# Kernel tuning notes

Measured on AMD Instinct MI355X. Metric: run time of the kernel, lower is better.

## Reference

```python
import jax, jax.numpy as jnp
import numpy as np
import math

HIDDEN = 128

def setup_inputs() -> dict:
    key = jax.random.key(0)
    k1, k2, k3 = jax.random.split(key, 3)
    X = jax.random.normal(k1, (4, 4096, HIDDEN), dtype=jnp.float32)
    # nn.Linear(hidden, 3*hidden): weight [3H, H], bias [3H]
    bound = 1.0 / math.sqrt(HIDDEN)
    W = jax.random.uniform(k2, (3 * HIDDEN, HIDDEN), minval=-bound, maxval=bound, dtype=jnp.float32)
    b = jax.random.uniform(k3, (3 * HIDDEN,), minval=-bound, maxval=bound, dtype=jnp.float32)
    return {"X": X, "W": W, "b": b}

def reference(X, W, b):
    H = X.shape[-1]
    # fused QKV projection: X @ W^T + b -> [B, S, 3H]
    qkv = jnp.einsum('bsh,oh->bso', X, W) + b
    Q, K, V = jnp.split(qkv, 3, axis=-1)
    # scaled dot-product attention (single head)
    scores = jnp.einsum('bqh,bkh->bqk', Q, K) / jnp.sqrt(jnp.asarray(H, X.dtype))
    weights = jax.nn.softmax(scores, axis=-1)
    return jnp.einsum('bqk,bkh->bqh', weights, V)
```

## Files before the change

### kernel.cpp

```cpp
#include <hip/hip_runtime.h>
#include <hip/hip_fp16.h>

typedef _Float16 f16;
typedef __attribute__((ext_vector_type(8))) _Float16 f16x8;
typedef __attribute__((ext_vector_type(4))) float f32x4;
typedef __attribute__((ext_vector_type(4))) unsigned int u32x4;
typedef __attribute__((ext_vector_type(2))) unsigned int u32x2;

#define BB 4
#define SS 4096
#define HH 128
#define SC2 0.12752462157076558f

union H2U { __half2 h; unsigned int u; };
union VU { u32x4 v; unsigned short s[8]; };
union F8U { u32x4 u; f16x8 h; };

#define LW 136
__global__ __launch_bounds__(256) void qkv_gemm(
    const float* __restrict__ X, const float* __restrict__ W,
    const float* __restrict__ bias, f16* __restrict__ Qh,
    f16* __restrict__ Kh, f16* __restrict__ Vh)
{
    __shared__ f16 sW[64 * LW];
    const int bx = blockIdx.x, by = blockIdx.y;
    const int t = threadIdx.x;
    const int w = t >> 6, lane = t & 63;
    const int c = lane & 15, quad = lane >> 4;

    f16x8 af[2][4];
    const int rbase = bx * 128 + w * 32;
#pragma unroll
    for (int mt = 0; mt < 2; ++mt) {
        const float* xr = X + (size_t)(rbase + mt * 16 + c) * HH + quad * 8;
#pragma unroll
        for (int kc = 0; kc < 4; ++kc) {
            float4 a = *(const float4*)(xr + kc * 32);
            float4 b = *(const float4*)(xr + kc * 32 + 4);
            H2U u0, u1, u2, u3;
            u0.h = __floats2half2_rn(a.x, a.y);
            u1.h = __floats2half2_rn(a.z, a.w);
            u2.h = __floats2half2_rn(b.x, b.y);
            u3.h = __floats2half2_rn(b.z, b.w);
            F8U pk; pk.u.x = u0.u; pk.u.y = u1.u; pk.u.z = u2.u; pk.u.w = u3.u;
            af[mt][kc] = pk.h;
        }
    }

    {
        const int r = t >> 2, q = t & 3;
        const float* src = W + (size_t)(by * 64 + r) * HH + q * 32;
        f16* dst = sW + r * LW + q * 32;
#pragma unroll
        for (int i = 0; i < 8; ++i) {
            float4 v = ((const float4*)src)[i];
            __half2 a = __floats2half2_rn(v.x, v.y);
            __half2 b = __floats2half2_rn(v.z, v.w);
            ((__half2*)dst)[2 * i] = a;
            ((__half2*)dst)[2 * i + 1] = b;
        }
    }
    __syncthreads();

    f32x4 acc[2][4];
#pragma unroll
    for (int mt = 0; mt < 2; ++mt)
#pragma unroll
        for (int nt = 0; nt < 4; ++nt) acc[mt][nt] = (f32x4)0.f;

#pragma unroll
    for (int kc = 0; kc < 4; ++kc) {
        f16x8 bf[4];
#pragma unroll
        for (int nt = 0; nt < 4; ++nt)
            bf[nt] = *(const f16x8*)&sW[(nt * 16 + c) * LW + kc * 32 + quad * 8];
#pragma unroll
        for (int mt = 0; mt < 2; ++mt)
#pragma unroll
            for (int nt = 0; nt < 4; ++nt)
                acc[mt][nt] = __builtin_amdgcn_mfma_f32_16x16x32_f16(af[mt][kc], bf[nt], acc[mt][nt], 0, 0, 0);
    }

    f16* outp = (by < 2) ? Qh : (by < 4) ? Kh : Vh;
    const int cbase = (by & 1) * 64;
#pragma unroll
    for (int nt = 0; nt < 4; ++nt) {
        const int cc = cbase + nt * 16 + c;
        const float bv = bias[by * 64 + nt * 16 + c];
#pragma unroll
        for (int mt = 0; mt < 2; ++mt) {
#pragma unroll
            for (int r = 0; r < 4; ++r) {
                const int row = rbase + mt * 16 + quad * 4 + r;
                outp[(size_t)row * HH + cc] = (f16)(acc[mt][nt][r] + bv);
            }
        }
    }
}

#define BM 64
#define BN 64
#define LK 136
#define LV 88
#define LP 88

__global__ __launch_bounds__(128, 2) void attn_mfma(
    const f16* __restrict__ Qh, const f16* __restrict__ Kh,
    const f16* __restrict__ Vh, float* __restrict__ out,
    float* __restrict__ Opart, float2* __restrict__ ml, int nsplit)
{
    __shared__ f16 sK[BN * LK];
    __shared__ f16 sVt[HH * LV];
    __shared__ f16 sP[2][32 * LP];

    const int bid = blockIdx.x;
    const int split = bid >> 8;
    const int inner = bid & 255;
    const int batch = inner & 3;
    const int qtile = inner >> 2;
    const int t = threadIdx.x;
    const int w = t >> 6, lane = t & 63;
    const int c = lane & 15, quad = lane >> 4;

    const int s0 = (64 * split) / nsplit;
    const int s1 = (64 * (split + 1)) / nsplit;
    const int nst = s1 - s0;
    const int kstart = s0 * BN;

    const f16* Qb = Qh + (size_t)batch * SS * HH;
    const f16* Kb = Kh + (size_t)batch * SS * HH;
    const f16* Vb = Vh + (size_t)batch * SS * HH;
    const int qbase = qtile * BM + w * 32;

    f16x8 qf[2][4];
#pragma unroll
    for (int qt = 0; qt < 2; ++qt)
#pragma unroll
        for (int kc = 0; kc < 4; ++kc)
            qf[qt][kc] = *(const f16x8*)(Qb + (size_t)(qbase + qt * 16 + c) * HH + kc * 32 + quad * 8);

    const int kr = t >> 1, kh = t & 1;
    const f16* kgp = Kb + (size_t)(kstart + kr) * HH + kh * 64;
    f16* ksp = sK + kr * LK + kh * 64;
    const int vkp = t & 31, vhq = t >> 5;
    const f16* vgp = Vb + (size_t)(kstart + 2 * vkp) * HH;

    u32x4 kbuf[8], vb0[4], vb1[4];
#pragma unroll
    for (int i = 0; i < 8; ++i) kbuf[i] = *(const u32x4*)(kgp + i * 8);
#pragma unroll
    for (int p = 0; p < 4; ++p) {
        const int hg = vhq * 4 + p;
        vb0[p] = *(const u32x4*)(vgp + hg * 8);
        vb1[p] = *(const u32x4*)(vgp + HH + hg * 8);
    }

    f32x4 oacc[2][8];
#pragma unroll
    for (int mt = 0; mt < 2; ++mt)
#pragma unroll
        for (int nt = 0; nt < 8; ++nt) oacc[mt][nt] = (f32x4)0.f;
    float m_[2] = {-1e30f, -1e30f}, l_[2] = {0.f, 0.f};

    for (int st = 0; st < nst; ++st) {
        __syncthreads();
#pragma unroll
        for (int i = 0; i < 8; ++i) *(u32x4*)(ksp + i * 8) = kbuf[i];
#pragma unroll
        for (int p = 0; p < 4; ++p) {
            const int hg = vhq * 4 + p;
            VU a, b; a.v = vb0[p]; b.v = vb1[p];
#pragma unroll
            for (int i = 0; i < 8; ++i) {
                unsigned int pk = (unsigned int)a.s[i] | ((unsigned int)b.s[i] << 16);
                *(unsigned int*)&sVt[(hg * 8 + i) * LV + 2 * vkp] = pk;
            }
        }
        __syncthreads();
        if (st + 1 < nst) {
            const f16* kg = kgp + (size_t)(st + 1) * BN * HH;
#pragma unroll
            for (int i = 0; i < 8; ++i) kbuf[i] = *(const u32x4*)(kg + i * 8);
            const f16* vg = vgp + (size_t)(st + 1) * BN * HH;
#pragma unroll
            for (int p = 0; p < 4; ++p) {
                const int hg = vhq * 4 + p;
                vb0[p] = *(const u32x4*)(vg + hg * 8);
                vb1[p] = *(const u32x4*)(vg + HH + hg * 8);
            }
        }

        f32x4 sacc[4][2];
#pragma unroll
        for (int km = 0; km < 4; ++km)
#pragma unroll
            for (int qt = 0; qt < 2; ++qt) sacc[km][qt] = (f32x4)0.f;
#pragma unroll
        for (int kc = 0; kc < 4; ++kc) {
#pragma unroll
            for (int km = 0; km < 4; ++km) {
                f16x8 kf = *(const f16x8*)&sK[(km * 16 + c) * LK + kc * 32 + quad * 8];
#pragma unroll
                for (int qt = 0; qt < 2; ++qt)
                    sacc[km][qt] = __builtin_amdgcn_mfma_f32_16x16x32_f16(kf, qf[qt][kc], sacc[km][qt], 0, 0, 0);
            }
        }

        float alpha_s[2];
#pragma unroll
        for (int qt = 0; qt < 2; ++qt) {
            float mx = sacc[0][qt][0];
#pragma unroll
            for (int km = 0; km < 4; ++km)
#pragma unroll
                for (int r = 0; r < 4; ++r) mx = fmaxf(mx, sacc[km][qt][r]);
            mx = fmaxf(mx, __shfl_xor(mx, 16));
            mx = fmaxf(mx, __shfl_xor(mx, 32));
            const float mn = fmaxf(m_[qt], mx);
            const float alpha = exp2f((m_[qt] - mn) * SC2);
            m_[qt] = mn;
            alpha_s[qt] = alpha;
            const float tb = mn * SC2;
            float ls = 0.f;
#pragma unroll
            for (int km = 0; km < 4; ++km) {
                float p0 = exp2f(sacc[km][qt][0] * SC2 - tb);
                float p1 = exp2f(sacc[km][qt][1] * SC2 - tb);
                float p2 = exp2f(sacc[km][qt][2] * SC2 - tb);
                float p3 = exp2f(sacc[km][qt][3] * SC2 - tb);
                ls += (p0 + p1) + (p2 + p3);
                H2U u0, u1;
                u0.h = __floats2half2_rn(p0, p1);
                u1.h = __floats2half2_rn(p2, p3);
                u32x2 pk; pk.x = u0.u; pk.y = u1.u;
                *(u32x2*)&sP[w][(qt * 16 + c) * LP + km * 16 + quad * 4] = pk;
            }
            ls += __shfl_xor(ls, 16);
            ls += __shfl_xor(ls, 32);
            l_[qt] = l_[qt] * alpha + ls;
        }

#pragma unroll
        for (int mt = 0; mt < 2; ++mt) {
            float av[4];
#pragma unroll
            for (int r = 0; r < 4; ++r)
                av[r] = __shfl(alpha_s[mt], quad * 4 + r);
#pragma unroll
            for (int nt = 0; nt < 8; ++nt)
#pragma unroll
                for (int r = 0; r < 4; ++r) oacc[mt][nt][r] *= av[r];
        }

#pragma unroll
        for (int kc2 = 0; kc2 < 2; ++kc2) {
            f16x8 pf[2];
#pragma unroll
            for (int mt = 0; mt < 2; ++mt)
                pf[mt] = *(const f16x8*)&sP[w][(mt * 16 + c) * LP + kc2 * 32 + quad * 8];
#pragma unroll
            for (int nt = 0; nt < 8; ++nt) {
                f16x8 vf = *(const f16x8*)&sVt[(nt * 16 + c) * LV + kc2 * 32 + quad * 8];
#pragma unroll
                for (int mt = 0; mt < 2; ++mt)
                    oacc[mt][nt] = __builtin_amdgcn_mfma_f32_16x16x32_f16(pf[mt], vf, oacc[mt][nt], 0, 0, 0);
            }
        }
    }

    float* Ob = (split == 0) ? out : (Opart + (size_t)(split - 1) * BB * SS * HH);
    float* ob = Ob + (size_t)(batch * SS + qbase) * HH;
    if (nsplit == 1) {
#pragma unroll
        for (int mt = 0; mt < 2; ++mt) {
            float lv[4];
#pragma unroll
            for (int r = 0; r < 4; ++r)
                lv[r] = 1.f / __shfl(l_[mt], quad * 4 + r);
#pragma unroll
            for (int r = 0; r < 4; ++r) {
                const int row = mt * 16 + quad * 4 + r;
#pragma unroll
                for (int nt = 0; nt < 8; ++nt)
                    ob[(size_t)row * HH + nt * 16 + c] = oacc[mt][nt][r] * lv[r];
            }
        }
    } else {
#pragma unroll
        for (int mt = 0; mt < 2; ++mt) {
#pragma unroll
            for (int r = 0; r < 4; ++r) {
                const int row = mt * 16 + quad * 4 + r;
#pragma unroll
                for (int nt = 0; nt < 8; ++nt)
                    ob[(size_t)row * HH + nt * 16 + c] = oacc[mt][nt][r];
            }
        }
        if (quad == 0) {
#pragma unroll
            for (int qt = 0; qt < 2; ++qt) {
                float2 v; v.x = m_[qt]; v.y = l_[qt];
                ml[((size_t)split * BB + batch) * SS + qbase + qt * 16 + c] = v;
            }
        }
    }
}

__global__ __launch_bounds__(256) void attn_merge(
    float* __restrict__ out, const float* __restrict__ Opart,
    const float2* __restrict__ ml, int nsplit)
{
    const int idx = blockIdx.x * 256 + threadIdx.x;
    const int chunk = idx & 31;
    const int q = (idx >> 5) & (SS - 1);
    const int b = idx >> 17;
    float m = -1e30f;
    for (int s = 0; s < nsplit; ++s)
        m = fmaxf(m, ml[((size_t)s * BB + b) * SS + q].x);
    float L = 0.f;
    float ax = 0.f, ay = 0.f, az = 0.f, aw = 0.f;
    for (int s = 0; s < nsplit; ++s) {
        float2 v = ml[((size_t)s * BB + b) * SS + q];
        const float wgt = exp2f((v.x - m) * SC2);
        L += v.y * wgt;
        const float* Op = (s == 0) ? out : (Opart + (size_t)(s - 1) * BB * SS * HH);
        float4 o = *(const float4*)(Op + ((size_t)b * SS + q) * HH + chunk * 4);
        ax += wgt * o.x; ay += wgt * o.y; az += wgt * o.z; aw += wgt * o.w;
    }
    const float inv = 1.f / L;
    float4 r; r.x = ax * inv; r.y = ay * inv; r.z = az * inv; r.w = aw * inv;
    *(float4*)(out + ((size_t)b * SS + q) * HH + chunk * 4) = r;
}

extern "C" void kernel_launch(void* const* d_in, const int* in_sizes, int n_in,
                              void* d_out, int out_size, void* d_ws, size_t ws_size,
                              hipStream_t stream) {
    const float* X = (const float*)d_in[0];
    const float* W = (const float*)d_in[1];
    const float* bias = (const float*)d_in[2];
    float* out = (float*)d_out;

    char* ws = (char*)d_ws;
    const size_t qkv_bytes = (size_t)3 * BB * SS * HH * sizeof(f16);
    const size_t o_bytes   = (size_t)BB * SS * HH * sizeof(float);
    const size_t ml_bytes  = (size_t)BB * SS * sizeof(float2);

    int S = 1;
    if (ws_size >= qkv_bytes + 2 * o_bytes + 3 * ml_bytes) S = 3;
    else if (ws_size >= qkv_bytes + 1 * o_bytes + 2 * ml_bytes) S = 2;

    f16* Qh = (f16*)ws;
    f16* Kh = Qh + (size_t)BB * SS * HH;
    f16* Vh = Kh + (size_t)BB * SS * HH;
    float* Opart = (float*)(ws + qkv_bytes);
    float2* ml = (float2*)(ws + qkv_bytes + (size_t)(S - 1) * o_bytes);

    qkv_gemm<<<dim3(128, 6), 256, 0, stream>>>(X, W, bias, Qh, Kh, Vh);
    attn_mfma<<<256 * S, 128, 0, stream>>>(Qh, Kh, Vh, out, Opart, ml, S);
    if (S > 1)
        attn_merge<<<BB * SS * (HH / 4) / 256, 256, 0, stream>>>(out, Opart, ml, S);
}
```

Before: 157.5 us.

## Enlarge attention query tile to 128 rows with 4 waves, widen QKV GEMM tile

The attention kernel now processes 128 query rows per block with 256 threads (four waves) instead of 64 rows with two waves. Each K/V tile staged in shared memory is therefore reused by twice as many queries, and the per-thread staging load is halved. The QKV GEMM block now computes a full 128-column output slice so X fragments are converted once per block instead of twice. The split-K count can rise to 4 to recover parallelism lost by the halved block count, at the cost of more partial output traffic in the merge step and higher shared memory per block.

Result: faster. 138.2 us (-12.3%).

```diff
diff --git a/kernel.cpp b/kernel.cpp
--- a/kernel.cpp
+++ b/kernel.cpp
@@ -22,7 +22,7 @@
     const float* __restrict__ bias, f16* __restrict__ Qh,
     f16* __restrict__ Kh, f16* __restrict__ Vh)
 {
-    __shared__ f16 sW[64 * LW];
+    __shared__ f16 sW[128 * LW];
     const int bx = blockIdx.x, by = blockIdx.y;
     const int t = threadIdx.x;
     const int w = t >> 6, lane = t & 63;
@@ -48,11 +48,11 @@
     }
 
     {
-        const int r = t >> 2, q = t & 3;
-        const float* src = W + (size_t)(by * 64 + r) * HH + q * 32;
-        f16* dst = sW + r * LW + q * 32;
-#pragma unroll
-        for (int i = 0; i < 8; ++i) {
+        const int r = t >> 1, h = t & 1;
+        const float* src = W + (size_t)(by * 128 + r) * HH + h * 64;
+        f16* dst = sW + r * LW + h * 64;
+#pragma unroll
+        for (int i = 0; i < 16; ++i) {
             float4 v = ((const float4*)src)[i];
             __half2 a = __floats2half2_rn(v.x, v.y);
             __half2 b = __floats2half2_rn(v.z, v.w);
@@ -62,31 +62,28 @@
     }
     __syncthreads();
 
-    f32x4 acc[2][4];
+    f32x4 acc[2][8];
 #pragma unroll
     for (int mt = 0; mt < 2; ++mt)
 #pragma unroll
-        for (int nt = 0; nt < 4; ++nt) acc[mt][nt] = (f32x4)0.f;
+        for (int nt = 0; nt < 8; ++nt) acc[mt][nt] = (f32x4)0.f;
 
 #pragma unroll
     for (int kc = 0; kc < 4; ++kc) {
-        f16x8 bf[4];
-#pragma unroll
-        for (int nt = 0; nt < 4; ++nt)
-            bf[nt] = *(const f16x8*)&sW[(nt * 16 + c) * LW + kc * 32 + quad * 8];
-#pragma unroll
-        for (int mt = 0; mt < 2; ++mt)
-#pragma unroll
-            for (int nt = 0; nt < 4; ++nt)
-                acc[mt][nt] = __builtin_amdgcn_mfma_f32_16x16x32_f16(af[mt][kc], bf[nt], acc[mt][nt], 0, 0, 0);
-    }
-
-    f16* outp = (by < 2) ? Qh : (by < 4) ? Kh : Vh;
-    const int cbase = (by & 1) * 64;
-#pragma unroll
-    for (int nt = 0; nt < 4; ++nt) {
-        const int cc = cbase + nt * 16 + c;
-        const float bv = bias[by * 64 + nt * 16 + c];
+#pragma unroll
+        for (int nt = 0; nt < 8; ++nt) {
+            f16x8 bf = *(const f16x8*)&sW[(nt * 16 + c) * LW + kc * 32 + quad * 8];
+#pragma unroll
+            for (int mt = 0; mt < 2; ++mt)
+                acc[mt][nt] = __builtin_amdgcn_mfma_f32_16x16x32_f16(af[mt][kc], bf, acc[mt][nt], 0, 0, 0);
+        }
+    }
+
+    f16* outp = (by == 0) ? Qh : (by == 1) ? Kh : Vh;
+#pragma unroll
+    for (int nt = 0; nt < 8; ++nt) {
+        const int cc = nt * 16 + c;
+        const float bv = bias[by * 128 + cc];
 #pragma unroll
         for (int mt = 0; mt < 2; ++mt) {
 #pragma unroll
@@ -98,24 +95,24 @@
     }
 }
 
-#define BM 64
+#define BM 128
 #define BN 64
 #define LK 136
-#define LV 88
-#define LP 88
-
-__global__ __launch_bounds__(128, 2) void attn_mfma(
+#define LV 72
+#define LP 72
+
+__global__ __launch_bounds__(256, 2) void attn_mfma(
     const f16* __restrict__ Qh, const f16* __restrict__ Kh,
     const f16* __restrict__ Vh, float* __restrict__ out,
     float* __restrict__ Opart, float2* __restrict__ ml, int nsplit)
 {
     __shared__ f16 sK[BN * LK];
     __shared__ f16 sVt[HH * LV];
-    __shared__ f16 sP[2][32 * LP];
+    __shared__ f16 sP[4][32 * LP];
 
     const int bid = blockIdx.x;
-    const int split = bid >> 8;
-    const int inner = bid & 255;
+    const int split = bid >> 7;
+    const int inner = bid & 127;
     const int batch = inner & 3;
     const int qtile = inner >> 2;
     const int t = threadIdx.x;
@@ -139,20 +136,19 @@
         for (int kc = 0; kc < 4; ++kc)
             qf[qt][kc] = *(const f16x8*)(Qb + (size_t)(qbase + qt * 16 + c) * HH + kc * 32 + quad * 8);
 
-    const int kr = t >> 1, kh = t & 1;
-    const f16* kgp = Kb + (size_t)(kstart + kr) * HH + kh * 64;
-    f16* ksp = sK + kr * LK + kh * 64;
+    const int kr = t >> 2, q4 = t & 3;
+    const f16* kgp = Kb + (size_t)(kstart + kr) * HH + q4 * 32;
+    f16* ksp = sK + kr * LK + q4 * 32;
     const int vkp = t & 31, vhq = t >> 5;
-    const f16* vgp = Vb + (size_t)(kstart + 2 * vkp) * HH;
-
-    u32x4 kbuf[8], vb0[4], vb1[4];
-#pragma unroll
-    for (int i = 0; i < 8; ++i) kbuf[i] = *(const u32x4*)(kgp + i * 8);
-#pragma unroll
-    for (int p = 0; p < 4; ++p) {
-        const int hg = vhq * 4 + p;
-        vb0[p] = *(const u32x4*)(vgp + hg * 8);
-        vb1[p] = *(const u32x4*)(vgp + HH + hg * 8);
+    const f16* vgp = Vb + (size_t)(kstart + 2 * vkp) * HH + vhq * 16;
+
+    u32x4 kbuf[4], vb0[2], vb1[2];
+#pragma unroll
+    for (int i = 0; i < 4; ++i) kbuf[i] = *(const u32x4*)(kgp + i * 8);
+#pragma unroll
+    for (int i = 0; i < 2; ++i) {
+        vb0[i] = *(const u32x4*)(vgp + i * 8);
+        vb1[i] = *(const u32x4*)(vgp + HH + i * 8);
     }
 
     f32x4 oacc[2][8];
@@ -165,28 +161,31 @@
     for (int st = 0; st < nst; ++st) {
         __syncthreads();
 #pragma unroll
-        for (int i = 0; i < 8; ++i) *(u32x4*)(ksp + i * 8) = kbuf[i];
-#pragma unroll
-        for (int p = 0; p < 4; ++p) {
-            const int hg = vhq * 4 + p;
-            VU a, b; a.v = vb0[p]; b.v = vb1[p];
-#pragma unroll
-            for (int i = 0; i < 8; ++i) {
-                unsigned int pk = (unsigned int)a.s[i] | ((unsigned int)b.s[i] << 16);
-                *(unsigned int*)&sVt[(hg * 8 + i) * LV + 2 * vkp] = pk;
+        for (int i = 0; i < 4; ++i) *(u32x4*)(ksp + i * 8) = kbuf[i];
+        {
+            VU a0, a1, b0, b1;
+            a0.v = vb0[0]; a1.v = vb0[1]; b0.v = vb1[0]; b1.v = vb1[1];
+#pragma unroll
+            for (int d = 0; d < 8; ++d) {
+                unsigned int pk = (unsigned int)a0.s[d] | ((unsigned int)b0.s[d] << 16);
+                *(unsigned int*)&sVt[(vhq * 16 + d) * LV + 2 * vkp] = pk;
+            }
+#pragma unroll
+            for (int d = 0; d < 8; ++d) {
+                unsigned int pk = (unsigned int)a1.s[d] | ((unsigned int)b1.s[d] << 16);
+                *(unsigned int*)&sVt[(vhq * 16 + 8 + d) * LV + 2 * vkp] = pk;
             }
         }
         __syncthreads();
         if (st + 1 < nst) {
             const f16* kg = kgp + (size_t)(st + 1) * BN * HH;
 #pragma unroll
-            for (int i = 0; i < 8; ++i) kbuf[i] = *(const u32x4*)(kg + i * 8);
+            for (int i = 0; i < 4; ++i) kbuf[i] = *(const u32x4*)(kg + i * 8);
             const f16* vg = vgp + (size_t)(st + 1) * BN * HH;
 #pragma unroll
-            for (int p = 0; p < 4; ++p) {
-                const int hg = vhq * 4 + p;
-                vb0[p] = *(const u32x4*)(vg + hg * 8);
-                vb1[p] = *(const u32x4*)(vg + HH + hg * 8);
+            for (int i = 0; i < 2; ++i) {
+                vb0[i] = *(const u32x4*)(vg + i * 8);
+                vb1[i] = *(const u32x4*)(vg + HH + i * 8);
             }
         }
 
@@ -346,8 +345,11 @@
     const size_t ml_bytes  = (size_t)BB * SS * sizeof(float2);
 
     int S = 1;
-    if (ws_size >= qkv_bytes + 2 * o_bytes + 3 * ml_bytes) S = 3;
-    else if (ws_size >= qkv_bytes + 1 * o_bytes + 2 * ml_bytes) S = 2;
+    for (int cand = 4; cand >= 2; --cand) {
+        if (ws_size >= qkv_bytes + (size_t)(cand - 1) * o_bytes + (size_t)cand * ml_bytes) {
+            S = cand; break;
+        }
+    }
 
     f16* Qh = (f16*)ws;
     f16* Kh = Qh + (size_t)BB * SS * HH;
@@ -355,8 +357,8 @@
     float* Opart = (float*)(ws + qkv_bytes);
     float2* ml = (float2*)(ws + qkv_bytes + (size_t)(S - 1) * o_bytes);
 
-    qkv_gemm<<<dim3(128, 6), 256, 0, stream>>>(X, W, bias, Qh, Kh, Vh);
-    attn_mfma<<<256 * S, 128, 0, stream>>>(Qh, Kh, Vh, out, Opart, ml, S);
+    qkv_gemm<<<dim3(128, 3), 256, 0, stream>>>(X, W, bias, Qh, Kh, Vh);
+    attn_mfma<<<128 * S, 256, 0, stream>>>(Qh, Kh, Vh, out, Opart, ml, S);
     if (S > 1)
         attn_merge<<<BB * SS * (HH / 4) / 256, 256, 0, stream>>>(out, Opart, ml, S);
 }
```
